# Kernel tuning notes

Hardware: AMD Instinct MI355X
Metric: run time of the kernel (lower is better)

The kernel has to match this reference:

```python
import jax, jax.numpy as jnp
import numpy as np

D_MODEL = 256
EXPERT_DIM = 512
NUM_EXPERTS = 8
TOP_K = 2
SEQ_LEN = 2048
BATCH = 2


def setup_inputs() -> dict:
    key = jax.random.key(0)
    ks = jax.random.split(key, 8)
    s = 0.02
    x = jax.random.normal(ks[0], (SEQ_LEN, BATCH, D_MODEL), dtype=jnp.float32)
    # gate: torch Linear(d_model, num_experts); store as [d, E] so logits = x @ Wg + bg
    Wg = jax.random.normal(ks[1], (D_MODEL, NUM_EXPERTS), dtype=jnp.float32) * s
    bg = jax.random.normal(ks[2], (NUM_EXPERTS,), dtype=jnp.float32) * s
    bias = jnp.zeros((NUM_EXPERTS,), dtype=jnp.float32)  # dynamic routing bias
    # experts: Linear(d, h) -> ReLU -> Linear(h, d), stacked over E
    W1 = jax.random.normal(ks[3], (NUM_EXPERTS, D_MODEL, EXPERT_DIM), dtype=jnp.float32) * s
    b1 = jax.random.normal(ks[4], (NUM_EXPERTS, EXPERT_DIM), dtype=jnp.float32) * s
    W2 = jax.random.normal(ks[5], (NUM_EXPERTS, EXPERT_DIM, D_MODEL), dtype=jnp.float32) * s
    b2 = jax.random.normal(ks[6], (NUM_EXPERTS, D_MODEL), dtype=jnp.float32) * s
    return {"x": x, "Wg": Wg, "bg": bg, "bias": bias, "W1": W1, "b1": b1, "W2": W2, "b2": b2}


def reference(x, Wg, bg, bias, W1, b1, W2, b2):
    # x: [seq, batch, d] -> flatten tokens
    x_flat = x.reshape(-1, D_MODEL)                      # [T, d]
    gate_logits = x_flat @ Wg + bg + bias                # [T, E]
    topk_vals, topk_idx = jax.lax.top_k(gate_logits, TOP_K)   # [T, K]
    # torch code subtracts the row max (topk_vals[:, :1], sorted desc) then softmaxes;
    # jax.nn.softmax is the same stable computation.
    topk_w = jax.nn.softmax(topk_vals, axis=-1)          # [T, K]
    # combine weights over experts: zero for unchosen experts -> exact same math
    # as the masked gather + scatter-add in the original loop.
    combine = (jax.nn.one_hot(topk_idx, NUM_EXPERTS, dtype=x.dtype)
               * topk_w[..., None]).sum(axis=1)          # [T, E]
    h = jax.nn.relu(jnp.einsum('td,edh->teh', x_flat, W1) + b1)   # [T, E, H]
    y = jnp.einsum('teh,ehd->ted', h, W2) + b2                     # [T, E, d]
    out = jnp.einsum('ted,te->td', y, combine)                     # [T, d]
    # dropout is identity in eval mode (p applied only in training)
    return out.reshape(x.shape)
```

## Files before the change

### kernel.cpp

```cpp
#include <hip/hip_runtime.h>
#include <hip/hip_bf16.h>
#include <math.h>

#define D_MODEL 256
#define EXPERT_DIM 512
#define NUM_EXPERTS 8
#define T_TOKENS 4096
#define TM 64
#define XS_LD 264

typedef unsigned short ushort_t;
typedef short short8_t __attribute__((ext_vector_type(8)));
typedef float f32x4 __attribute__((ext_vector_type(4)));

__device__ __forceinline__ ushort_t f2bf(float f) {
    unsigned int u = __float_as_uint(f);
    u += 0x7FFFu + ((u >> 16) & 1u);
    return (ushort_t)(u >> 16);
}

__global__ void zero_counts_kernel(int* __restrict__ counts)
{
    if (threadIdx.x < NUM_EXPERTS) counts[threadIdx.x] = 0;
}

__global__ __launch_bounds__(256) void prep_kernel(
    const float* __restrict__ x, const float* __restrict__ Wg,
    const float* __restrict__ bg, const float* __restrict__ bias,
    const float* __restrict__ W1, const float* __restrict__ W2,
    ushort_t* __restrict__ W1f, ushort_t* __restrict__ W2f,
    ushort_t* __restrict__ xb,
    int* __restrict__ counts, int* __restrict__ lists,
    float* __restrict__ wts, int* __restrict__ slots)
{
    __shared__ float xs[128][33];
    __shared__ float accbuf[128][9];
    __shared__ int lcount[NUM_EXPERTS];
    __shared__ int lbase[NUM_EXPERTS];

    const int tid = threadIdx.x;
    if (blockIdx.x < 32) {
        const int tbase = blockIdx.x * 128;
        const int tl = tid & 127;
        const int kh = tid >> 7;
        if (tid < NUM_EXPERTS) lcount[tid] = 0;
        float acc[NUM_EXPERTS];
#pragma unroll
        for (int e = 0; e < NUM_EXPERTS; ++e) acc[e] = 0.f;

        for (int kc = 0; kc < 8; ++kc) {
            __syncthreads();
#pragma unroll
            for (int it = 0; it < 4; ++it) {
                int pos = it * 256 + tid;
                int r = pos >> 3, c4 = pos & 7;
                const float* src = x + (size_t)(tbase + r) * D_MODEL + kc * 32 + c4 * 4;
                float4 v = *(const float4*)src;
                xs[r][c4 * 4 + 0] = v.x; xs[r][c4 * 4 + 1] = v.y;
                xs[r][c4 * 4 + 2] = v.z; xs[r][c4 * 4 + 3] = v.w;
                ushort4 o;
                o.x = f2bf(v.x); o.y = f2bf(v.y); o.z = f2bf(v.z); o.w = f2bf(v.w);
                *(ushort4*)&xb[(size_t)(tbase + r) * D_MODEL + kc * 32 + c4 * 4] = o;
            }
            __syncthreads();
            for (int k = kh * 16; k < kh * 16 + 16; ++k) {
                float xv = xs[tl][k];
                const float* wr = Wg + (kc * 32 + k) * NUM_EXPERTS;
#pragma unroll
                for (int e = 0; e < NUM_EXPERTS; ++e) acc[e] += xv * wr[e];
            }
        }
        __syncthreads();
        if (kh == 1) {
#pragma unroll
            for (int e = 0; e < NUM_EXPERTS; ++e) accbuf[tl][e] = acc[e];
        }
        __syncthreads();
        if (kh == 0) {
            float v0 = -3.0e38f, v1 = -3.0e38f; int i0 = 0, i1 = 0;
#pragma unroll
            for (int e = 0; e < NUM_EXPERTS; ++e) {
                float v = acc[e] + accbuf[tl][e] + bg[e] + bias[e];
                if (v > v0) { v1 = v0; i1 = i0; v0 = v; i0 = e; }
                else if (v > v1) { v1 = v; i1 = e; }
            }
            float e1 = __expf(v1 - v0);
            float inv = 1.f / (1.f + e1);
            float w0 = inv, w1 = e1 * inv;

            int p0 = atomicAdd(&lcount[i0], 1);
            int p1 = atomicAdd(&lcount[i1], 1);
            accbuf[tl][0] = w0; accbuf[tl][1] = w1;
            accbuf[tl][2] = __int_as_float(i0 * T_TOKENS + p0);
            accbuf[tl][3] = __int_as_float(i1 * T_TOKENS + p1);
        }
        __syncthreads();
        if (tid < NUM_EXPERTS) lbase[tid] = atomicAdd(&counts[tid], lcount[tid]);
        __syncthreads();
        if (kh == 0) {
            int t = tbase + tl;
            int s0 = __float_as_int(accbuf[tl][2]);
            int s1 = __float_as_int(accbuf[tl][3]);
            int q0 = s0 % T_TOKENS + lbase[s0 / T_TOKENS];
            int q1 = s1 % T_TOKENS + lbase[s1 / T_TOKENS];
            int i0 = s0 / T_TOKENS, i1 = s1 / T_TOKENS;
            lists[i0 * T_TOKENS + q0] = t;  wts[i0 * T_TOKENS + q0] = accbuf[tl][0];
            lists[i1 * T_TOKENS + q1] = t;  wts[i1 * T_TOKENS + q1] = accbuf[tl][1];
            slots[t * 2 + 0] = i0 * T_TOKENS + q0;
            slots[t * 2 + 1] = i1 * T_TOKENS + q1;
        }
    } else {
        int gid = (blockIdx.x - 32) * 256 + tid;
        bool isW2 = gid >= 131072;
        int idx = isW2 ? gid - 131072 : gid;
        int lane = idx & 63;
        int l15 = lane & 15, quad = lane >> 4;
        int ks = (idx >> 6) & 7;
        ushort_t o[8];
        if (!isW2) {
            int ntile = (idx >> 9) & 31, e = idx >> 14;
            int nn = ntile * 16 + l15;
            int k0 = ks * 32 + quad * 8;
            const float* s = W1 + ((size_t)e * D_MODEL + k0) * EXPERT_DIM + nn;
#pragma unroll
            for (int j = 0; j < 8; ++j) o[j] = f2bf(s[j * EXPERT_DIM]);
            *(int4*)(W1f + (size_t)idx * 8) = *(int4*)o;
        } else {
            int ntile = (idx >> 9) & 15, half = (idx >> 13) & 1, e = idx >> 14;
            int nn = ntile * 16 + l15;
            int k0 = half * 256 + ks * 32 + quad * 8;
            const float* s = W2 + ((size_t)e * EXPERT_DIM + k0) * D_MODEL + nn;
#pragma unroll
            for (int j = 0; j < 8; ++j) o[j] = f2bf(s[j * D_MODEL]);
            *(int4*)(W2f + (size_t)idx * 8) = *(int4*)o;
        }
    }
}

__global__ __launch_bounds__(256, 2) void moe_expert_mfma(
    const ushort_t* __restrict__ xb,
    const ushort_t* __restrict__ W1f, const float* __restrict__ b1,
    const ushort_t* __restrict__ W2f, const float* __restrict__ b2,
    const int* __restrict__ counts, const int* __restrict__ lists,
    const float* __restrict__ wts, float* __restrict__ ybuf)
{
    const int e = blockIdx.x;
    const int half = blockIdx.y;
    const int n = counts[e];
    const int base = blockIdx.z * TM;
    if (base >= n) return;
    const int m = min(TM, n - base);

    __shared__ ushort_t Xs[TM * XS_LD];
    __shared__ ushort_t Hs[TM * XS_LD];
    __shared__ int   toks[TM];
    __shared__ float wt_s[TM];

    const int tid = threadIdx.x;
    const int lane = tid & 63;
    const int w = tid >> 6;
    const int l15 = lane & 15;
    const int quad = lane >> 4;

    const ushort_t* W1p = W1f + (size_t)(e * 32 + half * 16 + w * 4) * 4096 + lane * 8;
    short8_t b1f[4][8];
#pragma unroll
    for (int nt = 0; nt < 4; ++nt)
#pragma unroll
        for (int ks = 0; ks < 8; ++ks)
            b1f[nt][ks] = *(const short8_t*)(W1p + nt * 4096 + ks * 512);

    if (tid < TM) {
        const int* lst = lists + e * T_TOKENS + base;
        const float* wr = wts + e * T_TOKENS + base;
        toks[tid] = (tid < m) ? lst[tid] : -1;
        wt_s[tid] = (tid < m) ? wr[tid] : 0.f;
    }
    __syncthreads();

    for (int c = tid; c < TM * 32; c += 256) {
        int r = c >> 5, c8 = c & 31;
        int tk = toks[r];
        int4 v = make_int4(0, 0, 0, 0);
        if (tk >= 0) v = *(const int4*)(xb + (size_t)tk * D_MODEL + c8 * 8);
        *(int4*)(Xs + r * XS_LD + c8 * 8) = v;
    }
    __syncthreads();

    float b1v[4];
#pragma unroll
    for (int nt = 0; nt < 4; ++nt)
        b1v[nt] = b1[e * EXPERT_DIM + half * 256 + w * 64 + nt * 16 + l15];

    f32x4 acc1[4][4] = {};
    for (int ks = 0; ks < 8; ++ks) {
        short8_t a[4];
#pragma unroll
        for (int mt = 0; mt < 4; ++mt)
            a[mt] = *(const short8_t*)(Xs + (mt * 16 + l15) * XS_LD + ks * 32 + quad * 8);
#pragma unroll
        for (int mt = 0; mt < 4; ++mt)
#pragma unroll
            for (int nt = 0; nt < 4; ++nt)
                acc1[mt][nt] = __builtin_amdgcn_mfma_f32_16x16x32_bf16(
                    a[mt], b1f[nt][ks], acc1[mt][nt], 0, 0, 0);
    }

    const ushort_t* W2p = W2f + (size_t)((e * 2 + half) * 16 + w * 4) * 4096 + lane * 8;
    short8_t b2f[4][8];
#pragma unroll
    for (int nt = 0; nt < 4; ++nt)
#pragma unroll
        for (int ks = 0; ks < 8; ++ks)
            b2f[nt][ks] = *(const short8_t*)(W2p + nt * 4096 + ks * 512);
    float b2v[4];
#pragma unroll
    for (int nt = 0; nt < 4; ++nt)
        b2v[nt] = half ? b2[e * D_MODEL + w * 64 + nt * 16 + l15] : 0.f;

#pragma unroll
    for (int mt = 0; mt < 4; ++mt)
#pragma unroll
        for (int nt = 0; nt < 4; ++nt)
#pragma unroll
            for (int r = 0; r < 4; ++r) {
                int row = mt * 16 + quad * 4 + r;
                int col = w * 64 + nt * 16 + l15;
                float h = fmaxf(acc1[mt][nt][r] + b1v[nt], 0.f);
                Hs[row * XS_LD + col] = f2bf(h);
            }
    __syncthreads();

    f32x4 acc2[4][4] = {};
    for (int ks = 0; ks < 8; ++ks) {
        short8_t a[4];
#pragma unroll
        for (int mt = 0; mt < 4; ++mt)
            a[mt] = *(const short8_t*)(Hs + (mt * 16 + l15) * XS_LD + ks * 32 + quad * 8);
#pragma unroll
        for (int mt = 0; mt < 4; ++mt)
#pragma unroll
            for (int nt = 0; nt < 4; ++nt)
                acc2[mt][nt] = __builtin_amdgcn_mfma_f32_16x16x32_bf16(
                    a[mt], b2f[nt][ks], acc2[mt][nt], 0, 0, 0);
    }

    float* yrow = ybuf + ((size_t)(half * NUM_EXPERTS + e) * T_TOKENS + base) * D_MODEL;
#pragma unroll
    for (int mt = 0; mt < 4; ++mt)
#pragma unroll
        for (int nt = 0; nt < 4; ++nt)
#pragma unroll
            for (int r = 0; r < 4; ++r) {
                int row = mt * 16 + quad * 4 + r;
                if (row < m) {
                    int col = w * 64 + nt * 16 + l15;
                    yrow[(size_t)row * D_MODEL + col] =
                        wt_s[row] * (acc2[mt][nt][r] + b2v[nt]);
                }
            }
}

__global__ __launch_bounds__(256) void combine_kernel(
    const int* __restrict__ slots, const float* __restrict__ ybuf,
    float* __restrict__ out)
{
    int gid = blockIdx.x * 256 + threadIdx.x;
    int t = gid >> 6, lane = gid & 63;
    int s0 = slots[t * 2 + 0];
    int s1 = slots[t * 2 + 1];
    const size_t H = (size_t)NUM_EXPERTS * T_TOKENS * D_MODEL;
    float4 a = ((const float4*)(ybuf + (size_t)s0 * D_MODEL))[lane];
    float4 b = ((const float4*)(ybuf + (size_t)s0 * D_MODEL + H))[lane];
    float4 c = ((const float4*)(ybuf + (size_t)s1 * D_MODEL))[lane];
    float4 d = ((const float4*)(ybuf + (size_t)s1 * D_MODEL + H))[lane];
    float4 r;
    r.x = a.x + b.x + c.x + d.x;
    r.y = a.y + b.y + c.y + d.y;
    r.z = a.z + b.z + c.z + d.z;
    r.w = a.w + b.w + c.w + d.w;
    ((float4*)(out + (size_t)t * D_MODEL))[lane] = r;
}

extern "C" void kernel_launch(void* const* d_in, const int* in_sizes, int n_in,
                              void* d_out, int out_size, void* d_ws, size_t ws_size,
                              hipStream_t stream)
{
    const float* x    = (const float*)d_in[0];
    const float* Wg   = (const float*)d_in[1];
    const float* bg   = (const float*)d_in[2];
    const float* bias = (const float*)d_in[3];
    const float* W1   = (const float*)d_in[4];
    const float* b1   = (const float*)d_in[5];
    const float* W2   = (const float*)d_in[6];
    const float* b2   = (const float*)d_in[7];
    float* out = (float*)d_out;

    char* ws = (char*)d_ws;
    int*      counts = (int*)ws;
    int*      lists  = (int*)(ws + 256);
    float*    wts    = (float*)(ws + 131328);
    int*      slots  = (int*)(ws + 262400);
    ushort_t* xb     = (ushort_t*)(ws + 524288);
    ushort_t* W1f    = (ushort_t*)(ws + 2621440);
    ushort_t* W2f    = (ushort_t*)(ws + 4718592);
    float*    ybuf   = (float*)(ws + 6815744);

    zero_counts_kernel<<<1, 64, 0, stream>>>(counts);

    prep_kernel<<<1056, 256, 0, stream>>>(
        x, Wg, bg, bias, W1, W2, W1f, W2f, xb, counts, lists, wts, slots);

    moe_expert_mfma<<<dim3(NUM_EXPERTS, 2, T_TOKENS / TM), 256, 0, stream>>>(
        xb, W1f, b1, W2f, b2, counts, lists, wts, ybuf);

    combine_kernel<<<T_TOKENS * 64 / 256, 256, 0, stream>>>(slots, ybuf, out);
}
```

Measured before the change: 115.9 us.

## Replace global atomic counts with per-block counts and stream expert weights

Each gating block now writes its per-expert counts to its own slot instead of doing a global atomicAdd, which removes the zero-counts kernel launch. The expert and combine kernels rebuild offsets with a wave prefix scan and a binary search. The expert kernel no longer holds all W1/W2 fragments in registers; it double-buffers them one k-step at a time and shares a single LDS buffer for X and H, raising the occupancy target from 2 to 3 blocks per CU. The cost is weight loads on the critical path inside the MFMA loop, plus extra scan work in each block.

```diff
diff --git a/kernel.cpp b/kernel.cpp
--- a/kernel.cpp
+++ b/kernel.cpp
@@ -7,6 +7,7 @@
 #define NUM_EXPERTS 8
 #define T_TOKENS 4096
 #define TM 64
+#define NGB 32
 #define XS_LD 264
 
 typedef unsigned short ushort_t;
@@ -17,11 +18,6 @@
     unsigned int u = __float_as_uint(f);
     u += 0x7FFFu + ((u >> 16) & 1u);
     return (ushort_t)(u >> 16);
-}
-
-__global__ void zero_counts_kernel(int* __restrict__ counts)
-{
-    if (threadIdx.x < NUM_EXPERTS) counts[threadIdx.x] = 0;
 }
 
 __global__ __launch_bounds__(256) void prep_kernel(
@@ -30,17 +26,17 @@
     const float* __restrict__ W1, const float* __restrict__ W2,
     ushort_t* __restrict__ W1f, ushort_t* __restrict__ W2f,
     ushort_t* __restrict__ xb,
-    int* __restrict__ counts, int* __restrict__ lists,
+    int* __restrict__ gcounts, int* __restrict__ lists,
     float* __restrict__ wts, int* __restrict__ slots)
 {
     __shared__ float xs[128][33];
     __shared__ float accbuf[128][9];
     __shared__ int lcount[NUM_EXPERTS];
-    __shared__ int lbase[NUM_EXPERTS];
 
     const int tid = threadIdx.x;
-    if (blockIdx.x < 32) {
-        const int tbase = blockIdx.x * 128;
+    if (blockIdx.x < NGB) {
+        const int gb = blockIdx.x;
+        const int tbase = gb * 128;
         const int tl = tid & 127;
         const int kh = tid >> 7;
         if (tid < NUM_EXPERTS) lcount[tid] = 0;
@@ -90,27 +86,17 @@
 
             int p0 = atomicAdd(&lcount[i0], 1);
             int p1 = atomicAdd(&lcount[i1], 1);
-            accbuf[tl][0] = w0; accbuf[tl][1] = w1;
-            accbuf[tl][2] = __int_as_float(i0 * T_TOKENS + p0);
-            accbuf[tl][3] = __int_as_float(i1 * T_TOKENS + p1);
+            int t = tbase + tl;
+            lists[i0 * T_TOKENS + gb * 128 + p0] = t;
+            wts  [i0 * T_TOKENS + gb * 128 + p0] = w0;
+            lists[i1 * T_TOKENS + gb * 128 + p1] = t;
+            wts  [i1 * T_TOKENS + gb * 128 + p1] = w1;
+            slots[t] = (i0 << 12 | gb << 7 | p0) | ((i1 << 12 | gb << 7 | p1) << 16);
         }
         __syncthreads();
-        if (tid < NUM_EXPERTS) lbase[tid] = atomicAdd(&counts[tid], lcount[tid]);
-        __syncthreads();
-        if (kh == 0) {
-            int t = tbase + tl;
-            int s0 = __float_as_int(accbuf[tl][2]);
-            int s1 = __float_as_int(accbuf[tl][3]);
-            int q0 = s0 % T_TOKENS + lbase[s0 / T_TOKENS];
-            int q1 = s1 % T_TOKENS + lbase[s1 / T_TOKENS];
-            int i0 = s0 / T_TOKENS, i1 = s1 / T_TOKENS;
-            lists[i0 * T_TOKENS + q0] = t;  wts[i0 * T_TOKENS + q0] = accbuf[tl][0];
-            lists[i1 * T_TOKENS + q1] = t;  wts[i1 * T_TOKENS + q1] = accbuf[tl][1];
-            slots[t * 2 + 0] = i0 * T_TOKENS + q0;
-            slots[t * 2 + 1] = i1 * T_TOKENS + q1;
-        }
+        if (tid < NUM_EXPERTS) gcounts[gb * NUM_EXPERTS + tid] = lcount[tid];
     } else {
-        int gid = (blockIdx.x - 32) * 256 + tid;
+        int gid = (blockIdx.x - NGB) * 256 + tid;
         bool isW2 = gid >= 131072;
         int idx = isW2 ? gid - 131072 : gid;
         int lane = idx & 63;
@@ -137,44 +123,54 @@
     }
 }
 
-__global__ __launch_bounds__(256, 2) void moe_expert_mfma(
+__global__ __launch_bounds__(256, 3) void moe_expert_mfma(
     const ushort_t* __restrict__ xb,
     const ushort_t* __restrict__ W1f, const float* __restrict__ b1,
     const ushort_t* __restrict__ W2f, const float* __restrict__ b2,
-    const int* __restrict__ counts, const int* __restrict__ lists,
+    const int* __restrict__ gcounts, const int* __restrict__ lists,
     const float* __restrict__ wts, float* __restrict__ ybuf)
 {
     const int e = blockIdx.x;
     const int half = blockIdx.y;
-    const int n = counts[e];
+
+    __shared__ ushort_t XH[TM * XS_LD];
+    __shared__ int cum[33];
+    __shared__ int   toks[TM];
+    __shared__ float wt_s[TM];
+
+    const int tid = threadIdx.x;
+    if (tid < 32) {
+        int v = gcounts[tid * NUM_EXPERTS + e];
+#pragma unroll
+        for (int s = 1; s < 32; s <<= 1) {
+            int u = __shfl_up(v, s, 32);
+            if (tid >= s) v += u;
+        }
+        cum[tid + 1] = v;
+        if (tid == 0) cum[0] = 0;
+    }
+    __syncthreads();
+    const int n = cum[32];
     const int base = blockIdx.z * TM;
     if (base >= n) return;
     const int m = min(TM, n - base);
 
-    __shared__ ushort_t Xs[TM * XS_LD];
-    __shared__ ushort_t Hs[TM * XS_LD];
-    __shared__ int   toks[TM];
-    __shared__ float wt_s[TM];
-
-    const int tid = threadIdx.x;
     const int lane = tid & 63;
     const int w = tid >> 6;
     const int l15 = lane & 15;
     const int quad = lane >> 4;
 
-    const ushort_t* W1p = W1f + (size_t)(e * 32 + half * 16 + w * 4) * 4096 + lane * 8;
-    short8_t b1f[4][8];
-#pragma unroll
-    for (int nt = 0; nt < 4; ++nt)
-#pragma unroll
-        for (int ks = 0; ks < 8; ++ks)
-            b1f[nt][ks] = *(const short8_t*)(W1p + nt * 4096 + ks * 512);
-
     if (tid < TM) {
-        const int* lst = lists + e * T_TOKENS + base;
-        const float* wr = wts + e * T_TOKENS + base;
-        toks[tid] = (tid < m) ? lst[tid] : -1;
-        wt_s[tid] = (tid < m) ? wr[tid] : 0.f;
+        int p = base + tid;
+        int tk = -1; float wv = 0.f;
+        if (p < n) {
+            int lo = 0;
+#pragma unroll
+            for (int s = 16; s >= 1; s >>= 1) if (cum[lo + s] <= p) lo += s;
+            int idx = e * T_TOKENS + lo * 128 + (p - cum[lo]);
+            tk = lists[idx]; wv = wts[idx];
+        }
+        toks[tid] = tk; wt_s[tid] = wv;
     }
     __syncthreads();
 
@@ -183,41 +179,54 @@
         int tk = toks[r];
         int4 v = make_int4(0, 0, 0, 0);
         if (tk >= 0) v = *(const int4*)(xb + (size_t)tk * D_MODEL + c8 * 8);
-        *(int4*)(Xs + r * XS_LD + c8 * 8) = v;
-    }
-    __syncthreads();
-
+        *(int4*)(XH + r * XS_LD + c8 * 8) = v;
+    }
+    __syncthreads();
+
+    const ushort_t* W1p = W1f + (size_t)(e * 32 + half * 16 + w * 4) * 4096 + lane * 8;
     float b1v[4];
 #pragma unroll
     for (int nt = 0; nt < 4; ++nt)
         b1v[nt] = b1[e * EXPERT_DIM + half * 256 + w * 64 + nt * 16 + l15];
 
     f32x4 acc1[4][4] = {};
+    short8_t bc[4];
+#pragma unroll
+    for (int nt = 0; nt < 4; ++nt) bc[nt] = *(const short8_t*)(W1p + nt * 4096);
+
     for (int ks = 0; ks < 8; ++ks) {
+        short8_t bn[4];
+        if (ks < 7) {
+#pragma unroll
+            for (int nt = 0; nt < 4; ++nt)
+                bn[nt] = *(const short8_t*)(W1p + nt * 4096 + (ks + 1) * 512);
+        }
         short8_t a[4];
 #pragma unroll
         for (int mt = 0; mt < 4; ++mt)
-            a[mt] = *(const short8_t*)(Xs + (mt * 16 + l15) * XS_LD + ks * 32 + quad * 8);
+            a[mt] = *(const short8_t*)(XH + (mt * 16 + l15) * XS_LD + ks * 32 + quad * 8);
 #pragma unroll
         for (int mt = 0; mt < 4; ++mt)
 #pragma unroll
             for (int nt = 0; nt < 4; ++nt)
                 acc1[mt][nt] = __builtin_amdgcn_mfma_f32_16x16x32_bf16(
-                    a[mt], b1f[nt][ks], acc1[mt][nt], 0, 0, 0);
+                    a[mt], bc[nt], acc1[mt][nt], 0, 0, 0);
+        if (ks < 7) {
+#pragma unroll
+            for (int nt = 0; nt < 4; ++nt) bc[nt] = bn[nt];
+        }
     }
 
     const ushort_t* W2p = W2f + (size_t)((e * 2 + half) * 16 + w * 4) * 4096 + lane * 8;
-    short8_t b2f[4][8];
-#pragma unroll
-    for (int nt = 0; nt < 4; ++nt)
-#pragma unroll
-        for (int ks = 0; ks < 8; ++ks)
-            b2f[nt][ks] = *(const short8_t*)(W2p + nt * 4096 + ks * 512);
+    short8_t bc2[4];
+#pragma unroll
+    for (int nt = 0; nt < 4; ++nt) bc2[nt] = *(const short8_t*)(W2p + nt * 4096);
     float b2v[4];
 #pragma unroll
     for (int nt = 0; nt < 4; ++nt)
         b2v[nt] = half ? b2[e * D_MODEL + w * 64 + nt * 16 + l15] : 0.f;
 
+    __syncthreads();
 #pragma unroll
     for (int mt = 0; mt < 4; ++mt)
 #pragma unroll
@@ -227,22 +236,32 @@
                 int row = mt * 16 + quad * 4 + r;
                 int col = w * 64 + nt * 16 + l15;
                 float h = fmaxf(acc1[mt][nt][r] + b1v[nt], 0.f);
-                Hs[row * XS_LD + col] = f2bf(h);
+                XH[row * XS_LD + col] = f2bf(h);
             }
     __syncthreads();
 
     f32x4 acc2[4][4] = {};
     for (int ks = 0; ks < 8; ++ks) {
+        short8_t bn2[4];
+        if (ks < 7) {
+#pragma unroll
+            for (int nt = 0; nt < 4; ++nt)
+                bn2[nt] = *(const short8_t*)(W2p + nt * 4096 + (ks + 1) * 512);
+        }
         short8_t a[4];
 #pragma unroll
         for (int mt = 0; mt < 4; ++mt)
-            a[mt] = *(const short8_t*)(Hs + (mt * 16 + l15) * XS_LD + ks * 32 + quad * 8);
+            a[mt] = *(const short8_t*)(XH + (mt * 16 + l15) * XS_LD + ks * 32 + quad * 8);
 #pragma unroll
         for (int mt = 0; mt < 4; ++mt)
 #pragma unroll
             for (int nt = 0; nt < 4; ++nt)
                 acc2[mt][nt] = __builtin_amdgcn_mfma_f32_16x16x32_bf16(
-                    a[mt], b2f[nt][ks], acc2[mt][nt], 0, 0, 0);
+                    a[mt], bc2[nt], acc2[mt][nt], 0, 0, 0);
+        if (ks < 7) {
+#pragma unroll
+            for (int nt = 0; nt < 4; ++nt) bc2[nt] = bn2[nt];
+        }
     }
 
     float* yrow = ybuf + ((size_t)(half * NUM_EXPERTS + e) * T_TOKENS + base) * D_MODEL;
@@ -262,18 +281,44 @@
 }
 
 __global__ __launch_bounds__(256) void combine_kernel(
-    const int* __restrict__ slots, const float* __restrict__ ybuf,
-    float* __restrict__ out)
+    const int* __restrict__ slots, const int* __restrict__ gcounts,
+    const float* __restrict__ ybuf, float* __restrict__ out)
 {
-    int gid = blockIdx.x * 256 + threadIdx.x;
-    int t = gid >> 6, lane = gid & 63;
-    int s0 = slots[t * 2 + 0];
-    int s1 = slots[t * 2 + 1];
+    __shared__ int cum8[NUM_EXPERTS][33];
+    const int tid = threadIdx.x;
+    const int lane = tid & 63;
+    const int wv = tid >> 6;
+    if (lane < 32) {
+#pragma unroll
+        for (int rpt = 0; rpt < 2; ++rpt) {
+            int e = wv + rpt * 4;
+            int v = gcounts[lane * NUM_EXPERTS + e];
+#pragma unroll
+            for (int s = 1; s < 32; s <<= 1) {
+                int u = __shfl_up(v, s, 32);
+                if (lane >= s) v += u;
+            }
+            cum8[e][lane + 1] = v;
+            if (lane == 0) cum8[e][0] = 0;
+        }
+    }
+    __syncthreads();
+
+    int gid = blockIdx.x * 256 + tid;
+    int t = gid >> 6;
+    int sl = slots[t];
+    int s0 = sl & 0xFFFF, s1 = (sl >> 16) & 0xFFFF;
+    int e0 = s0 >> 12, gb0 = (s0 >> 7) & 31, lp0 = s0 & 127;
+    int e1 = s1 >> 12, gb1 = (s1 >> 7) & 31, lp1 = s1 & 127;
+    int p0 = cum8[e0][gb0] + lp0;
+    int p1 = cum8[e1][gb1] + lp1;
     const size_t H = (size_t)NUM_EXPERTS * T_TOKENS * D_MODEL;
-    float4 a = ((const float4*)(ybuf + (size_t)s0 * D_MODEL))[lane];
-    float4 b = ((const float4*)(ybuf + (size_t)s0 * D_MODEL + H))[lane];
-    float4 c = ((const float4*)(ybuf + (size_t)s1 * D_MODEL))[lane];
-    float4 d = ((const float4*)(ybuf + (size_t)s1 * D_MODEL + H))[lane];
+    const float4* r0 = (const float4*)(ybuf + ((size_t)e0 * T_TOKENS + p0) * D_MODEL);
+    const float4* r1 = (const float4*)(ybuf + ((size_t)e1 * T_TOKENS + p1) * D_MODEL);
+    float4 a = r0[lane];
+    float4 b = *(const float4*)((const float*)(r0) + H + lane * 4);
+    float4 c = r1[lane];
+    float4 d = *(const float4*)((const float*)(r1) + H + lane * 4);
     float4 r;
     r.x = a.x + b.x + c.x + d.x;
     r.y = a.y + b.y + c.y + d.y;
@@ -297,22 +342,20 @@
     float* out = (float*)d_out;
 
     char* ws = (char*)d_ws;
-    int*      counts = (int*)ws;
-    int*      lists  = (int*)(ws + 256);
-    float*    wts    = (float*)(ws + 131328);
-    int*      slots  = (int*)(ws + 262400);
-    ushort_t* xb     = (ushort_t*)(ws + 524288);
-    ushort_t* W1f    = (ushort_t*)(ws + 2621440);
-    ushort_t* W2f    = (ushort_t*)(ws + 4718592);
-    float*    ybuf   = (float*)(ws + 6815744);
-
-    zero_counts_kernel<<<1, 64, 0, stream>>>(counts);
+    int*      gcounts = (int*)ws;
+    int*      lists   = (int*)(ws + 1024);
+    float*    wts     = (float*)(ws + 132096);
+    int*      slots   = (int*)(ws + 263168);
+    ushort_t* xb      = (ushort_t*)(ws + 524288);
+    ushort_t* W1f     = (ushort_t*)(ws + 2621440);
+    ushort_t* W2f     = (ushort_t*)(ws + 4718592);
+    float*    ybuf    = (float*)(ws + 6815744);
 
     prep_kernel<<<1056, 256, 0, stream>>>(
-        x, Wg, bg, bias, W1, W2, W1f, W2f, xb, counts, lists, wts, slots);
+        x, Wg, bg, bias, W1, W2, W1f, W2f, xb, gcounts, lists, wts, slots);
 
     moe_expert_mfma<<<dim3(NUM_EXPERTS, 2, T_TOKENS / TM), 256, 0, stream>>>(
-        xb, W1f, b1, W2f, b2, counts, lists, wts, ybuf);
-
-    combine_kernel<<<T_TOKENS * 64 / 256, 256, 0, stream>>>(slots, ybuf, out);
-}
+        xb, W1f, b1, W2f, b2, gcounts, lists, wts, ybuf);
+
+    combine_kernel<<<T_TOKENS * 64 / 256, 256, 0, stream>>>(slots, gcounts, ybuf, out);
+}
```

New measurement: 115.4 us. No clear change (-0.5%).
